# Kernel tuning notes

Hardware: AMD Instinct MI355X
Metric: run time of the kernel (lower is better)

The kernel has to match this reference:

```python
import jax, jax.numpy as jnp
import numpy as np

N = 100000
D = 128       # out_feats
QK = 32       # qk_dim
E = 1600000
K_HOPS = 7    # self._k


def setup_inputs() -> dict:
    key = jax.random.key(0)
    ks = jax.random.split(key, 10)
    h_train = jax.random.normal(ks[0], (N, D), dtype=jnp.float32)
    h_ori = jax.random.normal(ks[1], (N, D), dtype=jnp.float32)
    edge_index = jax.random.randint(ks[2], (2, E), 0, N, dtype=jnp.int64)
    s = 1.0 / np.sqrt(D)
    Wq = jax.random.uniform(ks[3], (D, QK), jnp.float32, -s, s)
    bq = jnp.zeros((QK,), jnp.float32)
    Wk = jax.random.uniform(ks[4], (D, QK), jnp.float32, -s, s)
    bk = jnp.zeros((QK,), jnp.float32)
    Wv = jax.random.uniform(ks[5], (D, D), jnp.float32, -s, s)
    bv = jnp.zeros((D,), jnp.float32)
    return {"h_train": h_train, "h_ori": h_ori, "edge_index": edge_index,
            "Wq": Wq, "bq": bq, "Wk": Wk, "bk": bk, "Wv": Wv, "bv": bv}


def _propagate(x, D_invsqrt, row, col):
    h = x * D_invsqrt
    m = h[row]                                   # [E, D] gather
    out = jax.ops.segment_sum(m, col, num_segments=N)
    return out * D_invsqrt


def reference(h_train, h_ori, edge_index, Wq, bq, Wk, bk, Wv, bv):
    x = h_train
    row, col = edge_index[0], edge_index[1]
    deg = jax.ops.segment_sum(jnp.ones((E,), x.dtype), row, num_segments=N)
    deg = jnp.clip(deg, 1.0)
    D_invsqrt = (deg ** -0.5)[:, None]           # [N,1]

    a_feat = x + _propagate(x, D_invsqrt, row, col)
    stack = [a_feat]
    for _ in range(K_HOPS):
        # unnLaplacian high pass: x - Ax_hat (dropout inactive in eval)
        x = x - _propagate(x, D_invsqrt, row, col)
        stack.append(x)
    L_stack = jnp.stack(stack, axis=1)           # [N, K, D]

    # FullAttention with global mean query
    q = h_ori @ Wq + bq                          # [N, QK]
    q_global = q.mean(axis=0)                    # [QK]
    keys = L_stack @ Wk + bk                     # [N, K, QK]
    values = L_stack @ Wv + bv                   # [N, K, D]
    scale = 1.0 / np.sqrt(D)                     # D = keys input last dim
    scores = jnp.einsum('q,nkq->nk', q_global, keys) * scale
    A = jax.nn.softmax(scores, axis=-1)          # [N, K]
    V = jnp.einsum('nk,nkd->nd', A, values)      # [N, D] (== sum over K dim)
    return V
```

## Files before the change

kernel.cpp:

```cpp
#include <hip/hip_runtime.h>
#include <hip/hip_fp16.h>
#include <math.h>

#define DFEAT 128
#define QKD 32
#define NPART 512

static inline size_t align256(size_t x) { return (x + 255) & ~size_t(255); }


__global__ void hist_kernel(const int* __restrict__ eidx, unsigned* __restrict__ cnt_row,
                            unsigned* __restrict__ bcount, int E, int nbuk) {
    __shared__ unsigned h[512];
    for (int i = threadIdx.x; i < 512; i += 256) h[i] = 0;
    __syncthreads();
    int base = blockIdx.x * 8192;
    int end = base + 8192; if (end > E) end = E;
    for (int i = base + threadIdx.x; i < end; i += 256) {
        atomicAdd(&cnt_row[eidx[i]], 1u);
        atomicAdd(&h[(unsigned)eidx[E + i] >> 8], 1u);
    }
    __syncthreads();
    for (int i = threadIdx.x; i < nbuk; i += 256)
        if (h[i]) atomicAdd(&bcount[i], h[i]);
}

__global__ void dinv_kernel(const unsigned* __restrict__ cnt_row, float* __restrict__ dinv,
                            float* __restrict__ dinv2, float* __restrict__ rec, int n) {
    int i = blockIdx.x * blockDim.x + threadIdx.x;
    if (i < n) {
        unsigned c = cnt_row[i];
        if (c < 1u) c = 1u;
        float fd = (float)c;
        float sq = sqrtf(fd);
        dinv[i] = 1.0f / sq;
        dinv2[i] = 1.0f / fd;
        rec[i] = sq;
    }
}


__global__ void bscan_kernel(const unsigned* __restrict__ bcount, unsigned* __restrict__ bbase,
                             unsigned* __restrict__ bcur, unsigned* __restrict__ colptr,
                             int nbuk, int n, int E) {
    __shared__ unsigned s[512];
    int t = threadIdx.x;
    unsigned v = (t < nbuk) ? bcount[t] : 0u;
    s[t] = v; __syncthreads();
    for (int off = 1; off < 512; off <<= 1) {
        unsigned u = (t >= off) ? s[t - off] : 0u;
        __syncthreads();
        s[t] += u;
        __syncthreads();
    }
    if (t < nbuk) { unsigned e = s[t] - v; bbase[t] = e; bcur[t] = e; }
    if (t == 0) { bbase[nbuk] = (unsigned)E; colptr[n] = (unsigned)E; }
}

__global__ void bscatter_kernel(const int* __restrict__ eidx, unsigned* __restrict__ bcur,
                                unsigned* __restrict__ pairs, int E) {
    __shared__ unsigned cnt[512];
    __shared__ unsigned cur[512];
    for (int i = threadIdx.x; i < 512; i += 256) cnt[i] = 0;
    __syncthreads();
    int base = blockIdx.x * 8192;
    int end = base + 8192; if (end > E) end = E;
    for (int i = base + threadIdx.x; i < end; i += 256)
        atomicAdd(&cnt[(unsigned)eidx[E + i] >> 8], 1u);
    __syncthreads();
    for (int i = threadIdx.x; i < 512; i += 256)
        cur[i] = cnt[i] ? atomicAdd(&bcur[i], cnt[i]) : 0u;
    __syncthreads();
    for (int i = base + threadIdx.x; i < end; i += 256) {
        int col = eidx[E + i];
        int row = eidx[i];
        unsigned pos = atomicAdd(&cur[(unsigned)col >> 8], 1u);
        pairs[pos] = ((unsigned)row << 8) | (unsigned)(col & 255);
    }
}

__global__ void bsort_kernel(const unsigned* __restrict__ pairs, const unsigned* __restrict__ bbase,
                             unsigned* __restrict__ colptr, int* __restrict__ rowlist, int n) {
    __shared__ unsigned s[256];
    __shared__ unsigned cur[256];
    int b = blockIdx.x;
    unsigned beg = bbase[b], end = bbase[b + 1];
    int t = threadIdx.x;
    s[t] = 0;
    __syncthreads();
    for (unsigned i = beg + t; i < end; i += 256)
        atomicAdd(&s[pairs[i] & 255u], 1u);
    __syncthreads();
    unsigned v = s[t];
    for (int off = 1; off < 256; off <<= 1) {
        unsigned u = (t >= off) ? s[t - off] : 0u;
        __syncthreads();
        s[t] += u;
        __syncthreads();
    }
    unsigned start = beg + (s[t] - v);
    cur[t] = start;
    int c = b * 256 + t;
    if (c < n) colptr[c] = start;
    __syncthreads();
    for (unsigned i = beg + t; i < end; i += 256) {
        unsigned pk = pairs[i];
        unsigned pos = atomicAdd(&cur[pk & 255u], 1u);
        rowlist[pos] = (int)(pk >> 8);
    }
}


__global__ void scale_cvt_kernel(const float* __restrict__ h, const float* __restrict__ dinv,
                                 __half2* __restrict__ y, int n64) {
    int i = blockIdx.x * blockDim.x + threadIdx.x;
    if (i < n64) {
        float d = dinv[i >> 6];
        float2 v = reinterpret_cast<const float2*>(h)[i];
        y[i] = __floats2half2_rn(d * v.x, d * v.y);
    }
}


__global__ void colmean_partial_kernel(const float* __restrict__ h, float* __restrict__ partialT, int n) {
    __shared__ float s[256];
    int t = threadIdx.x;
    int col = t & 127;
    int half = t >> 7;
    float acc = 0.f;
    for (int r = blockIdx.x * 2 + half; r < n; r += gridDim.x * 2)
        acc += h[(size_t)r * DFEAT + col];
    s[t] = acc; __syncthreads();
    if (t < 128) partialT[(size_t)t * NPART + blockIdx.x] = s[t] + s[t + 128];
}

__global__ void hbar_reduce_kernel(const float* __restrict__ partialT, float* __restrict__ hbar,
                                   float inv_n) {
    __shared__ float s[256];
    int c = blockIdx.x, t = threadIdx.x;
    float acc = partialT[(size_t)c * NPART + t] + partialT[(size_t)c * NPART + t + 256];
    s[t] = acc; __syncthreads();
    for (int off = 128; off > 0; off >>= 1) {
        if (t < off) s[t] += s[t + off];
        __syncthreads();
    }
    if (t == 0) hbar[c] = s[0] * inv_n;
}

__global__ void wkq_kernel(const float* __restrict__ hbar,
                           const float* __restrict__ Wq, const float* __restrict__ bq,
                           const float* __restrict__ Wk, const float* __restrict__ bk,
                           float* __restrict__ wkq_ck) {
    __shared__ float hb[DFEAT];
    __shared__ float pq[QKD][9];
    __shared__ float qg[QKD];
    int t = threadIdx.x;
    if (t < DFEAT) hb[t] = hbar[t];
    __syncthreads();
    int q = t & 31, ch = t >> 5;
    float a = 0.f;
    int d0 = ch * 16;
#pragma unroll
    for (int d = 0; d < 16; ++d) a += hb[d0 + d] * Wq[(d0 + d) * QKD + q];
    pq[q][ch] = a;
    __syncthreads();
    if (t < QKD) {
        float s = bq[t];
#pragma unroll
        for (int c2 = 0; c2 < 8; ++c2) s += pq[t][c2];
        qg[t] = s;
    }
    __syncthreads();
    if (t < DFEAT) {
        float w = 0.f;
#pragma unroll
        for (int k = 0; k < QKD; ++k) w += Wk[t * QKD + k] * qg[k];
        wkq_ck[t] = w;
    }
    if (t == 0) {
        float c = 0.f;
        for (int k = 0; k < QKD; ++k) c += bk[k] * qg[k];
        wkq_ck[DFEAT] = c;
    }
}


__device__ __forceinline__ void acc4(const uint2* __restrict__ yq, int r, int sl, float4& a) {
    uint2 v = yq[(size_t)r * 32 + sl];
    float2 f0 = __half22float2(*reinterpret_cast<const __half2*>(&v.x));
    float2 f1 = __half22float2(*reinterpret_cast<const __half2*>(&v.y));
    a.x += f0.x; a.y += f0.y; a.z += f1.x; a.w += f1.y;
}

__device__ __forceinline__ float hred(float s) {
    s += __shfl_xor(s, 1, 64);  s += __shfl_xor(s, 2, 64);  s += __shfl_xor(s, 4, 64);
    s += __shfl_xor(s, 8, 64);  s += __shfl_xor(s, 16, 64);
    return s;
}

__device__ __forceinline__ float4 gatherw(const uint2* __restrict__ y,
                                          const int* __restrict__ rowlist,
                                          unsigned beg, unsigned deg, unsigned mxd, int sl) {
    float4 a = make_float4(0.f, 0.f, 0.f, 0.f);
    unsigned i = 0;
    for (; i < (mxd & ~7u); i += 8) {
        unsigned rem = deg > i ? deg - i : 0;
        if (rem >= 8) {
            int4 q0 = *reinterpret_cast<const int4*>(&rowlist[beg + i]);
            int4 q1 = *reinterpret_cast<const int4*>(&rowlist[beg + i + 4]);
            acc4(y, q0.x, sl, a); acc4(y, q0.y, sl, a);
            acc4(y, q0.z, sl, a); acc4(y, q0.w, sl, a);
            acc4(y, q1.x, sl, a); acc4(y, q1.y, sl, a);
            acc4(y, q1.z, sl, a); acc4(y, q1.w, sl, a);
        } else if (rem >= 4) {
            int4 q = *reinterpret_cast<const int4*>(&rowlist[beg + i]);
            acc4(y, q.x, sl, a); acc4(y, q.y, sl, a);
            acc4(y, q.z, sl, a); acc4(y, q.w, sl, a);
            for (unsigned k = 4; k < rem; ++k) acc4(y, rowlist[beg + i + k], sl, a);
        } else if (rem) {
            for (unsigned k = 0; k < rem; ++k) acc4(y, rowlist[beg + i + k], sl, a);
        }
    }
    {
        unsigned rem = deg > i ? deg - i : 0;
        if (rem >= 4) {
            int4 q = *reinterpret_cast<const int4*>(&rowlist[beg + i]);
            acc4(y, q.x, sl, a); acc4(y, q.y, sl, a);
            acc4(y, q.z, sl, a); acc4(y, q.w, sl, a);
            for (unsigned k = 4; k < rem; ++k) acc4(y, rowlist[beg + i + k], sl, a);
        } else if (rem) {
            for (unsigned k = 0; k < rem; ++k) acc4(y, rowlist[beg + i + k], sl, a);
        }
    }
    return a;
}

__device__ __forceinline__ uint2 pack4(float a, float b, float c, float d) {
    uint2 r;
    __half2 h0 = __floats2half2_rn(a, b), h1 = __floats2half2_rn(c, d);
    r.x = *reinterpret_cast<unsigned*>(&h0);
    r.y = *reinterpret_cast<unsigned*>(&h1);
    return r;
}

__global__ void __launch_bounds__(256, 8)
prop0_kernel(const uint2* __restrict__ y0,
             const int* __restrict__ rowlist, const unsigned* __restrict__ colptr,
             const float* __restrict__ dinv, const float* __restrict__ rec,
             const float* __restrict__ wkq_ck,
             uint2* __restrict__ yout, uint2* __restrict__ U,
             float* __restrict__ m_run, float* __restrict__ den_run, int n) {
    int wid = threadIdx.x >> 6, lane = threadIdx.x & 63;
    int sub = lane >> 5, sl = lane & 31;
    int c = blockIdx.x * 8 + wid * 2 + sub;
    if (c >= n) c = n - 1;
    unsigned beg = colptr[c], end = colptr[c + 1];
    unsigned deg = end - beg;
    unsigned dego = __shfl_xor(deg, 32, 64);
    unsigned mxd = deg > dego ? deg : dego;
    float4 a = gatherw(y0, rowlist, beg, deg, mxd, sl);

    float dc = dinv[c], rc = rec[c];
    size_t off = (size_t)c * 32 + sl;
    uint2 bv = y0[off];
    float2 b0 = __half22float2(*reinterpret_cast<const __half2*>(&bv.x));
    float2 b1 = __half22float2(*reinterpret_cast<const __half2*>(&bv.y));
    float x0 = rc * b0.x, x1 = rc * b0.y, x2 = rc * b1.x, x3 = rc * b1.y;
    float p0 = dc * a.x, p1 = dc * a.y, p2 = dc * a.z, p3 = dc * a.w;
    float ad0 = x0 + p0, ad1 = x1 + p1, ad2 = x2 + p2, ad3 = x3 + p3;
    float sb0 = x0 - p0, sb1 = x1 - p1, sb2 = x2 - p2, sb3 = x3 - p3;
    yout[off] = pack4(dc * sb0, dc * sb1, dc * sb2, dc * sb3);

    const float scale = 0.08838834764831845f;
    float ck = wkq_ck[DFEAT];
    float4 wv = *reinterpret_cast<const float4*>(&wkq_ck[sl * 4]);
    float s0 = (hred(ad0 * wv.x + ad1 * wv.y + ad2 * wv.z + ad3 * wv.w) + ck) * scale;
    float s1 = (hred(sb0 * wv.x + sb1 * wv.y + sb2 * wv.z + sb3 * wv.w) + ck) * scale;
    float m = fmaxf(s0, s1);
    float e0 = expf(s0 - m), e1 = expf(s1 - m);
    U[off] = pack4(e0 * ad0 + e1 * sb0, e0 * ad1 + e1 * sb1,
                   e0 * ad2 + e1 * sb2, e0 * ad3 + e1 * sb3);
    if (sl == 0) { m_run[c] = m; den_run[c] = e0 + e1; }
}

__global__ void __launch_bounds__(256, 8)
prop_fused_kernel(const uint2* __restrict__ y, const int* __restrict__ rowlist,
                  const unsigned* __restrict__ colptr,
                  const float* __restrict__ dinv2, const float* __restrict__ rec,
                  const float* __restrict__ wkq_ck,
                  uint2* __restrict__ yout, uint2* __restrict__ U,
                  float* __restrict__ m_run, float* __restrict__ den_run, int n) {
    int wid = threadIdx.x >> 6, lane = threadIdx.x & 63;
    int sub = lane >> 5, sl = lane & 31;
    int c = blockIdx.x * 8 + wid * 2 + sub;
    if (c >= n) c = n - 1;
    unsigned beg = colptr[c], end = colptr[c + 1];
    unsigned deg = end - beg;
    unsigned dego = __shfl_xor(deg, 32, 64);
    unsigned mxd = deg > dego ? deg : dego;
    float4 a = gatherw(y, rowlist, beg, deg, mxd, sl);

    float d2 = dinv2[c], rc = rec[c];
    size_t off = (size_t)c * 32 + sl;
    uint2 bv = y[off];
    float2 b0 = __half22float2(*reinterpret_cast<const __half2*>(&bv.x));
    float2 b1 = __half22float2(*reinterpret_cast<const __half2*>(&bv.y));
    float y0 = b0.x - d2 * a.x, y1 = b0.y - d2 * a.y;
    float y2 = b1.x - d2 * a.z, y3 = b1.y - d2 * a.w;
    yout[off] = pack4(y0, y1, y2, y3);
    float x0 = rc * y0, x1 = rc * y1, x2 = rc * y2, x3 = rc * y3;

    const float scale = 0.08838834764831845f;
    float ck = wkq_ck[DFEAT];
    float4 wv = *reinterpret_cast<const float4*>(&wkq_ck[sl * 4]);
    float s = (hred(x0 * wv.x + x1 * wv.y + x2 * wv.z + x3 * wv.w) + ck) * scale;
    float m = m_run[c], den = den_run[c];
    float m2 = fmaxf(m, s);
    float alpha = expf(m - m2), beta = expf(s - m2);
    uint2 uv = U[off];
    float2 u0 = __half22float2(*reinterpret_cast<const __half2*>(&uv.x));
    float2 u1 = __half22float2(*reinterpret_cast<const __half2*>(&uv.y));
    U[off] = pack4(u0.x * alpha + beta * x0, u0.y * alpha + beta * x1,
                   u1.x * alpha + beta * x2, u1.y * alpha + beta * x3);
    if (sl == 0) { m_run[c] = m2; den_run[c] = den * alpha + beta; }
}


__global__ void final_gemm_kernel(const __half2* __restrict__ U, const float* __restrict__ den_run,
                                  const float* __restrict__ Wv, const float* __restrict__ bv,
                                  float* __restrict__ out, int n) {
    __shared__ float M[8][DFEAT];
    int wid = threadIdx.x >> 6, lane = threadIdx.x & 63;
    int base = blockIdx.x * 8;
    for (int u = 0; u < 2; ++u) {
        int nn = base + wid * 2 + u;
        if (nn < n) {
            float inv = 1.0f / den_run[nn];
            float2 v = __half22float2(U[(size_t)nn * 64 + lane]);
            *reinterpret_cast<float2*>(&M[wid * 2 + u][lane * 2]) = make_float2(v.x * inv, v.y * inv);
        }
    }
    __syncthreads();
    int j = threadIdx.x & 127, hgrp = threadIdx.x >> 7;
    float bvj = bv[j];
    float acc0 = bvj, acc1 = bvj, acc2 = bvj, acc3 = bvj;
    for (int d = 0; d < DFEAT; ++d) {
        float w = Wv[d * DFEAT + j];
        acc0 += M[hgrp * 4 + 0][d] * w;
        acc1 += M[hgrp * 4 + 1][d] * w;
        acc2 += M[hgrp * 4 + 2][d] * w;
        acc3 += M[hgrp * 4 + 3][d] * w;
    }
    int n0 = base + hgrp * 4;
    if (n0 + 0 < n) out[(size_t)(n0 + 0) * DFEAT + j] = acc0;
    if (n0 + 1 < n) out[(size_t)(n0 + 1) * DFEAT + j] = acc1;
    if (n0 + 2 < n) out[(size_t)(n0 + 2) * DFEAT + j] = acc2;
    if (n0 + 3 < n) out[(size_t)(n0 + 3) * DFEAT + j] = acc3;
}


extern "C" void kernel_launch(void* const* d_in, const int* in_sizes, int n_in,
                              void* d_out, int out_size, void* d_ws, size_t ws_size,
                              hipStream_t stream) {
    const float* h_train = (const float*)d_in[0];
    const float* h_ori   = (const float*)d_in[1];
    const int*   eidx    = (const int*)d_in[2];
    const float* Wq = (const float*)d_in[3];
    const float* bq = (const float*)d_in[4];
    const float* Wk = (const float*)d_in[5];
    const float* bk = (const float*)d_in[6];
    const float* Wv = (const float*)d_in[7];
    const float* bv = (const float*)d_in[8];
    float* out = (float*)d_out;

    const int n = in_sizes[0] / DFEAT;
    const int E = in_sizes[2] / 2;
    const int NBUK = (n + 255) >> 8;
    const int EB = (E + 8191) / 8192;
    size_t ND2 = (size_t)n * 64;

    if (NBUK > 512) return;

    char* p = (char*)d_ws;
    auto alloc = [&](size_t bytes) { char* r = p; p += align256(bytes); return r; };
    uint2*    yA       = (uint2*)   alloc(ND2 * 4);
    uint2*    yB       = (uint2*)   alloc(ND2 * 4);
    uint2*    U16      = (uint2*)   alloc(ND2 * 4);
    int*      rowlist  = (int*)     alloc((size_t)(E + 16) * 4);
    unsigned* pairs    = (unsigned*)alloc((size_t)E * 4);
    float*    dinv     = (float*)   alloc((size_t)n * 4);
    float*    dinv2    = (float*)   alloc((size_t)n * 4);
    float*    rec      = (float*)   alloc((size_t)n * 4);
    unsigned* cnt_row  = (unsigned*)alloc((size_t)n * 4);
    unsigned* colptr   = (unsigned*)alloc((size_t)(n + 1) * 4);
    unsigned* bcount   = (unsigned*)alloc((size_t)NBUK * 4);
    unsigned* bbase    = (unsigned*)alloc((size_t)(NBUK + 1) * 4);
    unsigned* bcur     = (unsigned*)alloc((size_t)NBUK * 4);
    float*    m_run    = (float*)   alloc((size_t)n * 4);
    float*    den_run  = (float*)   alloc((size_t)n * 4);
    float*    partialT = (float*)   alloc((size_t)NPART * DFEAT * 4);
    float*    hbar     = (float*)   alloc(DFEAT * 4);
    float*    wkq_ck   = (float*)   alloc((DFEAT + 1) * 4);
    if ((size_t)(p - (char*)d_ws) > ws_size) return;

    hipMemsetAsync(cnt_row, 0, (size_t)n * 4, stream);
    hipMemsetAsync(bcount, 0, (size_t)NBUK * 4, stream);

    hist_kernel<<<EB, 256, 0, stream>>>(eidx, cnt_row, bcount, E, NBUK);
    dinv_kernel<<<(n + 255) / 256, 256, 0, stream>>>(cnt_row, dinv, dinv2, rec, n);
    bscan_kernel<<<1, 512, 0, stream>>>(bcount, bbase, bcur, colptr, NBUK, n, E);
    bscatter_kernel<<<EB, 256, 0, stream>>>(eidx, bcur, pairs, E);
    bsort_kernel<<<NBUK, 256, 0, stream>>>(pairs, bbase, colptr, rowlist, n);

    scale_cvt_kernel<<<(n * 64 + 255) / 256, 256, 0, stream>>>(h_train, dinv, (__half2*)yA, n * 64);

    colmean_partial_kernel<<<NPART, 256, 0, stream>>>(h_ori, partialT, n);
    hbar_reduce_kernel<<<DFEAT, 256, 0, stream>>>(partialT, hbar, 1.0f / (float)n);
    wkq_kernel<<<1, 256, 0, stream>>>(hbar, Wq, bq, Wk, bk, wkq_ck);

    prop0_kernel<<<(n + 7) / 8, 256, 0, stream>>>(yA, rowlist, colptr, dinv, rec, wkq_ck,
                                                  yB, U16, m_run, den_run, n);
    uint2* xin = yB; uint2* xout = yA;
    for (int t = 2; t <= 7; ++t) {
        prop_fused_kernel<<<(n + 7) / 8, 256, 0, stream>>>(xin, rowlist, colptr, dinv2, rec, wkq_ck,
                                                           xout, U16, m_run, den_run, n);
        uint2* tmp = xin; xin = xout; xout = tmp;
    }

    final_gemm_kernel<<<(n + 7) / 8, 256, 0, stream>>>((const __half2*)U16, den_run, Wv, bv, out, n);
}
```

Measured before the change: 742.0 us.

## Replace scalar final Wv GEMM with fp16 MFMA kernel using swizzled LDS weights

```diff
diff --git a/kernel.cpp b/kernel.cpp
--- a/kernel.cpp
+++ b/kernel.cpp
@@ -5,6 +5,9 @@
 #define DFEAT 128
 #define QKD 32
 #define NPART 512
+
+typedef _Float16 half8 __attribute__((ext_vector_type(8)));
+typedef float floatx4 __attribute__((ext_vector_type(4)));
 
 static inline size_t align256(size_t x) { return (x + 255) & ~size_t(255); }
 
@@ -118,6 +121,15 @@
         float d = dinv[i >> 6];
         float2 v = reinterpret_cast<const float2*>(h)[i];
         y[i] = __floats2half2_rn(d * v.x, d * v.y);
+    }
+}
+
+
+__global__ void cvt_wvt_kernel(const float* __restrict__ Wv, _Float16* __restrict__ wvt) {
+    int t = blockIdx.x * blockDim.x + threadIdx.x;
+    if (t < DFEAT * DFEAT) {
+        int j = t >> 7, d = t & 127;
+        wvt[t] = (_Float16)Wv[d * DFEAT + j];
     }
 }
 
@@ -262,9 +274,9 @@
 
     float dc = dinv[c], rc = rec[c];
     size_t off = (size_t)c * 32 + sl;
-    uint2 bv = y0[off];
-    float2 b0 = __half22float2(*reinterpret_cast<const __half2*>(&bv.x));
-    float2 b1 = __half22float2(*reinterpret_cast<const __half2*>(&bv.y));
+    uint2 bvv = y0[off];
+    float2 b0 = __half22float2(*reinterpret_cast<const __half2*>(&bvv.x));
+    float2 b1 = __half22float2(*reinterpret_cast<const __half2*>(&bvv.y));
     float x0 = rc * b0.x, x1 = rc * b0.y, x2 = rc * b1.x, x3 = rc * b1.y;
     float p0 = dc * a.x, p1 = dc * a.y, p2 = dc * a.z, p3 = dc * a.w;
     float ad0 = x0 + p0, ad1 = x1 + p1, ad2 = x2 + p2, ad3 = x3 + p3;
@@ -302,9 +314,9 @@
 
     float d2 = dinv2[c], rc = rec[c];
     size_t off = (size_t)c * 32 + sl;
-    uint2 bv = y[off];
-    float2 b0 = __half22float2(*reinterpret_cast<const __half2*>(&bv.x));
-    float2 b1 = __half22float2(*reinterpret_cast<const __half2*>(&bv.y));
+    uint2 bvv = y[off];
+    float2 b0 = __half22float2(*reinterpret_cast<const __half2*>(&bvv.x));
+    float2 b1 = __half22float2(*reinterpret_cast<const __half2*>(&bvv.y));
     float y0 = b0.x - d2 * a.x, y1 = b0.y - d2 * a.y;
     float y2 = b1.x - d2 * a.z, y3 = b1.y - d2 * a.w;
     yout[off] = pack4(y0, y1, y2, y3);
@@ -326,36 +338,58 @@
 }
 
 
-__global__ void final_gemm_kernel(const __half2* __restrict__ U, const float* __restrict__ den_run,
-                                  const float* __restrict__ Wv, const float* __restrict__ bv,
-                                  float* __restrict__ out, int n) {
-    __shared__ float M[8][DFEAT];
-    int wid = threadIdx.x >> 6, lane = threadIdx.x & 63;
-    int base = blockIdx.x * 8;
-    for (int u = 0; u < 2; ++u) {
-        int nn = base + wid * 2 + u;
-        if (nn < n) {
-            float inv = 1.0f / den_run[nn];
-            float2 v = __half22float2(U[(size_t)nn * 64 + lane]);
-            *reinterpret_cast<float2*>(&M[wid * 2 + u][lane * 2]) = make_float2(v.x * inv, v.y * inv);
+__global__ void __launch_bounds__(256, 4)
+final_mfma_kernel(const _Float16* __restrict__ Uh, const float* __restrict__ den,
+                  const unsigned* __restrict__ wvtU, const float* __restrict__ bv,
+                  float* __restrict__ out, int n) {
+    __shared__ unsigned wT[8192];
+    for (int i = threadIdx.x; i < 8192; i += 256) {
+        int col = i >> 6, inner = i & 63;
+        wT[col * 64 + (inner ^ ((col & 7) << 2))] = wvtU[i];
+    }
+    __syncthreads();
+    int wave = threadIdx.x >> 6, lane = threadIdx.x & 63;
+    int row0 = blockIdx.x * 64 + wave * 16;
+    int l15 = lane & 15, grp = lane >> 4;
+    int kgrp = grp * 8;
+    int arow = row0 + l15; if (arow >= n) arow = n - 1;
+    const _Float16* aptr = Uh + (size_t)arow * DFEAT + kgrp;
+    half8 af[4];
+    af[0] = *(const half8*)(aptr);
+    af[1] = *(const half8*)(aptr + 32);
+    af[2] = *(const half8*)(aptr + 64);
+    af[3] = *(const half8*)(aptr + 96);
+    const _Float16* wTh = (const _Float16*)wT;
+    floatx4 acc[8];
+#pragma unroll
+    for (int ct = 0; ct < 8; ++ct) acc[ct] = (floatx4){0.f, 0.f, 0.f, 0.f};
+#pragma unroll
+    for (int kt = 0; kt < 4; ++kt) {
+        int kbase = kt * 32 + kgrp;
+#pragma unroll
+        for (int ct = 0; ct < 8; ++ct) {
+            int col = ct * 16 + l15;
+            half8 bf = *(const half8*)&wTh[col * 128 + (kbase ^ ((col & 7) << 3))];
+            acc[ct] = __builtin_amdgcn_mfma_f32_16x16x32_f16(af[kt], bf, acc[ct], 0, 0, 0);
         }
     }
-    __syncthreads();
-    int j = threadIdx.x & 127, hgrp = threadIdx.x >> 7;
-    float bvj = bv[j];
-    float acc0 = bvj, acc1 = bvj, acc2 = bvj, acc3 = bvj;
-    for (int d = 0; d < DFEAT; ++d) {
-        float w = Wv[d * DFEAT + j];
-        acc0 += M[hgrp * 4 + 0][d] * w;
-        acc1 += M[hgrp * 4 + 1][d] * w;
-        acc2 += M[hgrp * 4 + 2][d] * w;
-        acc3 += M[hgrp * 4 + 3][d] * w;
-    }
-    int n0 = base + hgrp * 4;
-    if (n0 + 0 < n) out[(size_t)(n0 + 0) * DFEAT + j] = acc0;
-    if (n0 + 1 < n) out[(size_t)(n0 + 1) * DFEAT + j] = acc1;
-    if (n0 + 2 < n) out[(size_t)(n0 + 2) * DFEAT + j] = acc2;
-    if (n0 + 3 < n) out[(size_t)(n0 + 3) * DFEAT + j] = acc3;
+    int m0 = row0 + grp * 4;
+    float invd[4];
+#pragma unroll
+    for (int r = 0; r < 4; ++r) {
+        int gr = m0 + r;
+        invd[r] = 1.0f / den[gr < n ? gr : (n - 1)];
+    }
+#pragma unroll
+    for (int ct = 0; ct < 8; ++ct) {
+        int col = ct * 16 + l15;
+        float bvc = bv[col];
+#pragma unroll
+        for (int r = 0; r < 4; ++r) {
+            int gr = m0 + r;
+            if (gr < n) out[(size_t)gr * DFEAT + col] = acc[ct][r] * invd[r] + bvc;
+        }
+    }
 }
 
 
@@ -401,6 +435,7 @@
     float*    partialT = (float*)   alloc((size_t)NPART * DFEAT * 4);
     float*    hbar     = (float*)   alloc(DFEAT * 4);
     float*    wkq_ck   = (float*)   alloc((DFEAT + 1) * 4);
+    _Float16* wvt      = (_Float16*)alloc((size_t)DFEAT * DFEAT * 2);
     if ((size_t)(p - (char*)d_ws) > ws_size) return;
 
     hipMemsetAsync(cnt_row, 0, (size_t)n * 4, stream);
@@ -413,6 +448,7 @@
     bsort_kernel<<<NBUK, 256, 0, stream>>>(pairs, bbase, colptr, rowlist, n);
 
     scale_cvt_kernel<<<(n * 64 + 255) / 256, 256, 0, stream>>>(h_train, dinv, (__half2*)yA, n * 64);
+    cvt_wvt_kernel<<<64, 256, 0, stream>>>(Wv, wvt);
 
     colmean_partial_kernel<<<NPART, 256, 0, stream>>>(h_ori, partialT, n);
     hbar_reduce_kernel<<<DFEAT, 256, 0, stream>>>(partialT, hbar, 1.0f / (float)n);
@@ -427,5 +463,6 @@
         uint2* tmp = xin; xin = xout; xout = tmp;
     }
 
-    final_gemm_kernel<<<(n + 7) / 8, 256, 0, stream>>>((const __half2*)U16, den_run, Wv, bv, out, n);
-}
+    final_mfma_kernel<<<(n + 63) / 64, 256, 0, stream>>>((const _Float16*)U16, den_run,
+                                                         (const unsigned*)wvt, bv, out, n);
+}
```

After: 685.3 us. 1.08x faster.
